# Kernel tuning notes

Measured on AMD Instinct MI355X. Metric: run time of the kernel, lower is better.

## Reference

```python
import jax, jax.numpy as jnp
import numpy as np

N, E, B = 20000, 320000, 64
IN_DIM, HID, HEADS, NGF = 128, 64, 4, 9
NEG_SLOPE = 0.2
SET2SET_STEPS = 3


def _gat_conv(x, src, dst, W, a_src, a_dst, b, n):
    # PyG GATConv (eval mode): h = xW split into heads, edge score =
    # LeakyReLU(a_src.h[src] + a_dst.h[dst]), softmax over edges per dst node,
    # weighted scatter-sum of h[src], heads concatenated, + bias.
    H, C = a_src.shape
    h = (x @ W).reshape(n, H, C)                       # [N,H,C]
    s = jnp.sum(h * a_src, axis=-1)                    # [N,H]
    d = jnp.sum(h * a_dst, axis=-1)                    # [N,H]
    e = jax.nn.leaky_relu(s[src] + d[dst], NEG_SLOPE)  # [E,H]
    emax = jax.ops.segment_max(e, dst, num_segments=n)
    ex = jnp.exp(e - emax[dst])
    denom = jax.ops.segment_sum(ex, dst, num_segments=n)
    alpha = ex / (denom[dst] + 1e-16)                  # [E,H]
    out = jax.ops.segment_sum(h[src] * alpha[..., None], dst, num_segments=n)
    return out.reshape(n, H * C) + b


def _set2set(x, batch, Wih, Whh, bih, bhh, n_graphs):
    # Set2Set pooling: LSTM(q_star) -> attention over nodes per graph -> readout.
    d = x.shape[1]
    h = jnp.zeros((n_graphs, d), x.dtype)
    c = jnp.zeros((n_graphs, d), x.dtype)
    q_star = jnp.zeros((n_graphs, 2 * d), x.dtype)
    for _ in range(SET2SET_STEPS):
        gates = q_star @ Wih.T + bih + h @ Whh.T + bhh   # [B,4d], torch gate order i,f,g,o
        i, f, g, o = jnp.split(gates, 4, axis=1)
        c = jax.nn.sigmoid(f) * c + jax.nn.sigmoid(i) * jnp.tanh(g)
        h = jax.nn.sigmoid(o) * jnp.tanh(c)
        q = h                                            # [B,d]
        e = jnp.sum(x * q[batch], axis=-1)               # [N]
        emax = jax.ops.segment_max(e, batch, num_segments=n_graphs)
        a = jnp.exp(e - emax[batch])
        a = a / (jax.ops.segment_sum(a, batch, num_segments=n_graphs)[batch] + 1e-16)
        r = jax.ops.segment_sum(a[:, None] * x, batch, num_segments=n_graphs)  # [B,d]
        q_star = jnp.concatenate([q, r], axis=1)
    return q_star


def setup_inputs() -> dict:
    key = jax.random.key(0)
    ks = jax.random.split(key, 20)
    sc = 0.1
    inp = {
        "x": jax.random.normal(ks[0], (N, IN_DIM), jnp.float32),
        "edge_index": jax.random.randint(ks[1], (2, E), 0, N, dtype=jnp.int32),
        "batch": jnp.sort(jax.random.randint(ks[2], (N,), 0, B, dtype=jnp.int32)),
        "graph_features": jax.random.normal(ks[3], (B, NGF), jnp.float32),
        "W1": sc * jax.random.normal(ks[4], (IN_DIM, HEADS * HID), jnp.float32),
        "a_src1": sc * jax.random.normal(ks[5], (HEADS, HID), jnp.float32),
        "a_dst1": sc * jax.random.normal(ks[6], (HEADS, HID), jnp.float32),
        "b1": jnp.zeros((HEADS * HID,), jnp.float32),
        "W2": sc * jax.random.normal(ks[7], (HEADS * HID, HEADS * HID), jnp.float32),
        "a_src2": sc * jax.random.normal(ks[8], (HEADS, HID), jnp.float32),
        "a_dst2": sc * jax.random.normal(ks[9], (HEADS, HID), jnp.float32),
        "b2": jnp.zeros((HEADS * HID,), jnp.float32),
        "W3": sc * jax.random.normal(ks[10], (HEADS * HID, 2 * HID), jnp.float32),
        "a_src3": sc * jax.random.normal(ks[11], (1, 2 * HID), jnp.float32),
        "a_dst3": sc * jax.random.normal(ks[12], (1, 2 * HID), jnp.float32),
        "b3": jnp.zeros((2 * HID,), jnp.float32),
        "Wih": sc * jax.random.normal(ks[13], (4 * 2 * HID, 4 * HID), jnp.float32),
        "Whh": sc * jax.random.normal(ks[14], (4 * 2 * HID, 2 * HID), jnp.float32),
        "bih": jnp.zeros((4 * 2 * HID,), jnp.float32),
        "bhh": jnp.zeros((4 * 2 * HID,), jnp.float32),
        "gW1": sc * jax.random.normal(ks[15], (NGF, HID), jnp.float32),
        "gb1": jnp.zeros((HID,), jnp.float32),
        "gW2": sc * jax.random.normal(ks[16], (HID, HID // 2), jnp.float32),
        "gb2": jnp.zeros((HID // 2,), jnp.float32),
        "mW1": sc * jax.random.normal(ks[17], (2 * (2 * HID) + HID // 2, 128), jnp.float32),
        "mb1": jnp.zeros((128,), jnp.float32),
        "mW2": sc * jax.random.normal(ks[18], (128, 4), jnp.float32),
        "mb2": jnp.zeros((4,), jnp.float32),
    }
    return inp


def reference(x, edge_index, batch, graph_features,
              W1, a_src1, a_dst1, b1,
              W2, a_src2, a_dst2, b2,
              W3, a_src3, a_dst3, b3,
              Wih, Whh, bih, bhh,
              gW1, gb1, gW2, gb2,
              mW1, mb1, mW2, mb2):
    n = x.shape[0]
    # PyG GATConv default add_self_loops=True
    loops = jnp.arange(n, dtype=edge_index.dtype)
    src = jnp.concatenate([edge_index[0], loops])
    dst = jnp.concatenate([edge_index[1], loops])
    h = jax.nn.elu(_gat_conv(x, src, dst, W1, a_src1, a_dst1, b1, n))
    h = jax.nn.elu(_gat_conv(h, src, dst, W2, a_src2, a_dst2, b2, n))
    h = jax.nn.elu(_gat_conv(h, src, dst, W3, a_src3, a_dst3, b3, n))
    pooled = _set2set(h, batch, Wih, Whh, bih, bhh, B)              # [B, 256]
    gf = jax.nn.relu(graph_features @ gW1 + gb1) @ gW2 + gb2        # [B, 32]
    z = jnp.concatenate([pooled, gf], axis=1)                       # [B, 288]
    scores = jax.nn.relu(z @ mW1 + mb1) @ mW2 + mb2                 # [B, 4]
    return scores
```

## Files before the change

### kernel.cpp

```cpp
#include <hip/hip_runtime.h>
#include <hip/hip_bf16.h>
#include <math.h>

#define NEG_SLOPE 0.2f

typedef __attribute__((ext_vector_type(8))) short bf16x8;
typedef __attribute__((ext_vector_type(4))) float f32x4;

__device__ __forceinline__ float sigmoidf(float x){ return 1.f/(1.f+expf(-x)); }

__device__ __forceinline__ unsigned pack_split(float v){
  __hip_bfloat16 hi = __float2bfloat16(v);
  float rem = v - __bfloat162float(hi);
  __hip_bfloat16 lo = __float2bfloat16(rem);
  unsigned short uh = __builtin_bit_cast(unsigned short, hi);
  unsigned short ul = __builtin_bit_cast(unsigned short, lo);
  return (unsigned)uh | ((unsigned)ul << 16);
}
__device__ __forceinline__ unsigned short bf16of(float v){
  __hip_bfloat16 h = __float2bfloat16(v);
  return __builtin_bit_cast(unsigned short, h);
}

__global__ void init_kernel(int* counts, int* gstart, int* gend,
                            float* rsum, float* lsum,
                            int* pad1, int* pad2, int npadints,
                            const float* __restrict__ W1, unsigned* __restrict__ WT1,
                            const float* __restrict__ W2, unsigned* __restrict__ WT2,
                            const float* __restrict__ W3, unsigned* __restrict__ WT3,
                            int n, int b){
  int i = blockIdx.x*blockDim.x + threadIdx.x;
  if (i < n) counts[i] = 0;
  if (i < b){ gstart[i] = 0; gend[i] = 0; }
  if (i < 3*b*128) rsum[i] = 0.f;
  if (i < 3*b) lsum[i] = 0.f;
  if (i < npadints){ pad1[i] = 0; pad2[i] = 0; }
  if (i < 128*256){
    int k = i>>8, c = i&255;
    WT1[(size_t)c*128 + k] = pack_split(W1[i]);
  }
  if (i < 256*256){
    int k = i>>8, c = i&255;
    WT2[(size_t)c*256 + k] = pack_split(W2[i]);
  }
  if (i < 256*128){
    int k = i>>7, c = i&127;
    WT3[(size_t)c*256 + k] = pack_split(W3[i]);
  }
}

__global__ void build_kernel(const int* __restrict__ ei, const int* __restrict__ batch,
                             int* counts, int* gstart, int* gend, int E, int n){
  int i = blockIdx.x*blockDim.x + threadIdx.x;
  if (i < E) atomicAdd(&counts[ei[E+i]], 1);
  if (i < n){
    int b = batch[i];
    if (i == 0 || batch[i-1] != b) gstart[b] = i;
    if (i == n-1 || batch[i+1] != b) gend[b] = i+1;
  }
}

__global__ void scan_kernel(const int* __restrict__ counts, int* offs, int* cursor, int n){
  const int T = 1024;
  int tid = threadIdx.x;
  int chunk = (n + T - 1)/T;
  int base = tid*chunk;
  int local = 0;
  for (int i=0;i<chunk;i++){ int idx=base+i; if (idx<n) local += counts[idx]; }
  __shared__ int ss[T];
  ss[tid]=local; __syncthreads();
  for (int off=1; off<T; off<<=1){
    int v = (tid>=off)? ss[tid-off] : 0;
    __syncthreads();
    ss[tid]+=v;
    __syncthreads();
  }
  int run = ss[tid]-local;
  for (int i=0;i<chunk;i++){
    int idx=base+i;
    if (idx<n){ offs[idx]=run; cursor[idx]=run; run += counts[idx]; }
  }
  if (tid==T-1) offs[n]=run;
}

__global__ void fill_kernel(const int* __restrict__ ei, int* cursor, int* csr, int E){
  int i = blockIdx.x*blockDim.x + threadIdx.x;
  if (i<E){
    int dst = ei[E+i];
    int pos = atomicAdd(&cursor[dst],1);
    csr[pos] = ei[i];
  }
}

template<bool AF32>
__global__ __launch_bounds__(256) void gemm_bf16(
    const void* __restrict__ Aptr, const short* __restrict__ BT,
    float* __restrict__ C, unsigned short* __restrict__ Cb16,
    int M, int Ktot, int N){
  __shared__ short As[64][72];
  __shared__ short Bs[128][72];
  int tid = threadIdx.x;
  int wave = tid>>6, lane = tid&63;
  int quad = lane>>4, l16 = lane&15;
  int bm = blockIdx.x*64, bn = blockIdx.y*128;
  f32x4 acc[8];
  #pragma unroll
  for (int i=0;i<8;i++) acc[i] = (f32x4){0.f,0.f,0.f,0.f};
  int rr = tid>>3;
  int seg = (tid&7)*8;
  int4 ra[2], rb[4];
  auto loadAB = [&](int k0){
    if (AF32){
      const float* A = (const float*)Aptr;
      int Kf = Ktot>>1;
      int fo = (k0+seg)>>1;
      #pragma unroll
      for (int p=0;p<2;p++){
        int row = bm + p*32 + rr;
        float4 v = make_float4(0.f,0.f,0.f,0.f);
        if (row < M) v = *(const float4*)(A + (size_t)row*Kf + fo);
        ra[p] = make_int4((int)pack_split(v.x),(int)pack_split(v.y),
                          (int)pack_split(v.z),(int)pack_split(v.w));
      }
    } else {
      const short* A = (const short*)Aptr;
      #pragma unroll
      for (int p=0;p<2;p++)
        ra[p] = *(const int4*)(A + (size_t)(bm + p*32 + rr)*Ktot + k0 + seg);
    }
    #pragma unroll
    for (int p=0;p<4;p++)
      rb[p] = *(const int4*)(BT + (size_t)(bn + p*32 + rr)*Ktot + k0 + seg);
  };
  loadAB(0);
  for (int k0=0; k0<Ktot; k0+=64){
    __syncthreads();
    #pragma unroll
    for (int p=0;p<2;p++) *(int4*)&As[p*32+rr][seg] = ra[p];
    #pragma unroll
    for (int p=0;p<4;p++) *(int4*)&Bs[p*32+rr][seg] = rb[p];
    __syncthreads();
    if (k0+64 < Ktot) loadAB(k0+64);
    #pragma unroll
    for (int kk=0;kk<2;kk++){
      bf16x8 af = *(bf16x8*)&As[wave*16 + l16][kk*32 + quad*8];
      #pragma unroll
      for (int nf=0;nf<8;nf++){
        bf16x8 bfv = *(bf16x8*)&Bs[nf*16 + l16][kk*32 + quad*8];
        acc[nf] = __builtin_amdgcn_mfma_f32_16x16x32_bf16(af, bfv, acc[nf], 0,0,0);
      }
    }
  }
  #pragma unroll
  for (int r=0;r<4;r++){
    int row = bm + wave*16 + quad*4 + r;
    if (row < M){
      #pragma unroll
      for (int nf=0;nf<8;nf++){
        float v = acc[nf][r];
        int col = bn + nf*16 + l16;
        C[(size_t)row*N + col] = v;
        Cb16[(size_t)row*N + col] = bf16of(v);
      }
    }
  }
}

template<int H, int C>
__global__ void sd_kernel(const float* __restrict__ h, const float* __restrict__ asrc,
                          const float* __restrict__ adst, float* __restrict__ s,
                          float* __restrict__ d, int n_nodes){
  constexpr int HC = H*C;
  int wave = threadIdx.x >> 6, lane = threadIdx.x & 63;
  int n = blockIdx.x*4 + wave;
  if (n >= n_nodes) return;
  if (HC == 256){
    float4 hv = *reinterpret_cast<const float4*>(h + (size_t)n*256 + lane*4);
    float4 av = *reinterpret_cast<const float4*>(asrc + lane*4);
    float4 dv = *reinterpret_cast<const float4*>(adst + lane*4);
    float ps = hv.x*av.x + hv.y*av.y + hv.z*av.z + hv.w*av.w;
    float pd = hv.x*dv.x + hv.y*dv.y + hv.z*dv.z + hv.w*dv.w;
    #pragma unroll
    for (int off=1; off<16; off<<=1){ ps += __shfl_xor(ps,off); pd += __shfl_xor(pd,off); }
    if ((lane&15)==0){
      int head = lane>>4;
      s[n*4+head]=ps; d[n*4+head]=pd;
    }
  } else {
    if (lane < 32){
      float4 hv = *reinterpret_cast<const float4*>(h + (size_t)n*128 + lane*4);
      float4 av = *reinterpret_cast<const float4*>(asrc + lane*4);
      float4 dv = *reinterpret_cast<const float4*>(adst + lane*4);
      float ps = hv.x*av.x + hv.y*av.y + hv.z*av.z + hv.w*av.w;
      float pd = hv.x*dv.x + hv.y*dv.y + hv.z*dv.z + hv.w*dv.w;
      #pragma unroll
      for (int off=1; off<32; off<<=1){ ps += __shfl_xor(ps,off); pd += __shfl_xor(pd,off); }
      if (lane==0){ s[n]=ps; d[n]=pd; }
    }
  }
}

template<int H, int C, bool SPLIT>
__global__ __launch_bounds__(256) void agg_kernel(
    const unsigned short* __restrict__ hb, const float* __restrict__ s,
    const float* __restrict__ d, const int* __restrict__ offs,
    const int* __restrict__ csr, const float* __restrict__ bias,
    float* __restrict__ yf, unsigned* __restrict__ ys, int n_nodes){
  constexpr int HC = H*C;
  constexpr int VEC = HC/64;
  int n = blockIdx.x;
  int tid = threadIdx.x;
  int wave = tid>>6, lane = tid&63;
  __shared__ float sdst[H];
  __shared__ float sl[H];
  __shared__ float sw[64*H];
  __shared__ int ssrc[64];
  __shared__ float facc[4][HC];
  if (tid < H) sdst[tid] = d[n*H+tid];
  int start = offs[n];
  int cnt = offs[n+1]-start;
  int cnt1 = cnt+1;
  __syncthreads();
  float acc[VEC] = {};
  float lp[H];
  #pragma unroll
  for (int h=0;h<H;h++) lp[h]=0.f;
  for (int base=0; base<cnt1; base+=64){
    int nchunk = min(64, cnt1-base);
    if (tid < nchunk){
      int i = base+tid;
      int src = (i==cnt) ? n : csr[start+i];
      ssrc[tid]=src;
      if (H == 4){
        float4 sv = *reinterpret_cast<const float4*>(s + (size_t)src*4);
        float ev[4] = {sv.x, sv.y, sv.z, sv.w};
        #pragma unroll
        for (int h=0;h<4;h++){
          float e = ev[h] + sdst[h];
          e = e>=0.f ? e : NEG_SLOPE*e;
          float w = expf(e);
          sw[tid*4+h]=w;
          lp[h]+=w;
        }
      } else {
        float e = s[src] + sdst[0];
        e = e>=0.f ? e : NEG_SLOPE*e;
        float w = expf(e);
        sw[tid]=w;
        lp[0]+=w;
      }
    }
    __syncthreads();
    for (int j=wave; j<nchunk; j+=4){
      int src = ssrc[j];
      const unsigned short* hp = hb + (size_t)src*HC + lane*VEC;
      if (VEC == 4){
        float wt = sw[j*H + (lane>>4)];
        int2 hv = *reinterpret_cast<const int2*>(hp);
        acc[0] += wt*__uint_as_float(((unsigned)hv.x & 0xFFFFu) << 16);
        acc[1] += wt*__uint_as_float((unsigned)hv.x & 0xFFFF0000u);
        acc[2] += wt*__uint_as_float(((unsigned)hv.y & 0xFFFFu) << 16);
        acc[3] += wt*__uint_as_float((unsigned)hv.y & 0xFFFF0000u);
      } else {
        float wt = sw[j];
        unsigned hv = *reinterpret_cast<const unsigned*>(hp);
        acc[0] += wt*__uint_as_float((hv & 0xFFFFu) << 16);
        acc[1] += wt*__uint_as_float(hv & 0xFFFF0000u);
      }
    }
    __syncthreads();
  }
  if (wave==0){
    #pragma unroll
    for (int off=32; off; off>>=1)
      #pragma unroll
      for (int h=0;h<H;h++) lp[h] += __shfl_down(lp[h],off);
    if (lane==0)
      #pragma unroll
      for (int h=0;h<H;h++) sl[h]=lp[h];
  }
  #pragma unroll
  for (int v=0;v<VEC;v++) facc[wave][lane*VEC+v] = acc[v];
  __syncthreads();
  if (tid < HC){
    float a = facc[0][tid]+facc[1][tid]+facc[2][tid]+facc[3][tid];
    int head = tid / C;
    float o = a/(sl[head]+1e-16f) + bias[tid];
    o = o>0.f ? o : expm1f(o);
    if (SPLIT){
      ys[(size_t)n*HC + tid] = pack_split(o);
    } else {
      yf[(size_t)n*HC + tid] = o;
    }
  }
}

__global__ __launch_bounds__(256) void read_kernel(
    const float* __restrict__ x, const float* __restrict__ q,
    const int* __restrict__ batch,
    float* __restrict__ rsum, float* __restrict__ lsum, int N){
  int tid = threadIdx.x;
  int wave = tid>>6, lane = tid&63;
  int c0 = blockIdx.x*32;
  if (c0 >= N) return;
  __shared__ float ws[32];
  __shared__ int gb[32];
  if (tid < 32 && c0+tid < N) gb[tid] = batch[c0+tid];
  __syncthreads();
  #pragma unroll
  for (int j=0;j<8;j++){
    int k = wave*8 + j;
    int i = c0 + k;
    if (i < N){
      int g = gb[k];
      float2 xv = *reinterpret_cast<const float2*>(x + (size_t)i*128 + lane*2);
      float2 qv = *reinterpret_cast<const float2*>(q + (size_t)g*128 + lane*2);
      float p = xv.x*qv.x + xv.y*qv.y;
      #pragma unroll
      for (int off=32; off; off>>=1) p += __shfl_down(p, off);
      if (lane==0) ws[k] = expf(p);
    }
  }
  __syncthreads();
  if (tid < 128){
    int col = tid;
    int endi = min(c0+32, N);
    int curg = gb[0];
    float acc = 0.f, lacc = 0.f;
    for (int i=c0; i<endi; ++i){
      int g = gb[i-c0];
      if (g != curg){
        atomicAdd(&rsum[curg*128+col], acc);
        if (col==0) atomicAdd(&lsum[curg], lacc);
        acc = 0.f; lacc = 0.f; curg = g;
      }
      float w = ws[i-c0];
      acc += w * x[(size_t)i*128+col];
      lacc += w;
    }
    atomicAdd(&rsum[curg*128+col], acc);
    if (col==0) atomicAdd(&lsum[curg], lacc);
  }
}

template<int STEP>
__global__ __launch_bounds__(256) void s2s_step_kernel(
    const float* __restrict__ rsum, const float* __restrict__ lsum,
    float* __restrict__ hc, float* __restrict__ qbuf,
    const float* __restrict__ Wih, const float* __restrict__ Whh,
    const float* __restrict__ bih, const float* __restrict__ bhh,
    const float* __restrict__ gfeat,
    const float* __restrict__ gW1, const float* __restrict__ gb1,
    const float* __restrict__ gW2, const float* __restrict__ gb2,
    const float* __restrict__ mW1, const float* __restrict__ mb1,
    const float* __restrict__ mW2, const float* __restrict__ mb2,
    float* __restrict__ out, int B){
  int b = blockIdx.x, tid = threadIdx.x;
  __shared__ float qs[256];

  if (STEP > 0){
    if (tid < 128){
      const float* rs = rsum + (size_t)(STEP-1)*B*128 + (size_t)b*128;
      float ls = lsum[(STEP-1)*B + b];
      qs[tid]     = qbuf[b*128+tid];
      qs[128+tid] = rs[tid] / (ls + 1e-16f);
    }
    __syncthreads();
  }

  if (STEP < 3){
    __shared__ float hs[128], gsh[512];
    if (STEP > 0){ if (tid<128) hs[tid] = hc[(size_t)b*128+tid]; }
    __syncthreads();
    #pragma unroll
    for (int p=0;p<2;p++){
      int j = tid + p*256;
      float a = bih[j] + bhh[j];
      if (STEP > 0){
        const float* wi = Wih + (size_t)j*256;
        for (int k=0;k<256;k+=4)
          a += qs[k]*wi[k] + qs[k+1]*wi[k+1] + qs[k+2]*wi[k+2] + qs[k+3]*wi[k+3];
        const float* wh = Whh + (size_t)j*128;
        for (int k=0;k<128;k+=4)
          a += hs[k]*wh[k] + hs[k+1]*wh[k+1] + hs[k+2]*wh[k+2] + hs[k+3]*wh[k+3];
      }
      gsh[j] = a;
    }
    __syncthreads();
    if (tid < 128){
      float cprev = (STEP==0) ? 0.f : hc[(size_t)(B+b)*128+tid];
      float ig = sigmoidf(gsh[tid]);
      float fg = sigmoidf(gsh[128+tid]);
      float gg = tanhf(gsh[256+tid]);
      float og = sigmoidf(gsh[384+tid]);
      float c2 = fg*cprev + ig*gg;
      float h2 = og*tanhf(c2);
      hc[(size_t)b*128+tid] = h2;
      hc[(size_t)(B+b)*128+tid] = c2;
      qbuf[b*128+tid] = h2;
    }
  } else {
    __shared__ float z[288], gf1[64], hid[128];
    z[tid] = qs[tid];
    if (tid < 64){
      float a = gb1[tid];
      for (int k=0;k<9;k++) a += gfeat[b*9+k]*gW1[k*64+tid];
      gf1[tid] = a>0.f ? a : 0.f;
    }
    __syncthreads();
    if (tid < 32){
      float a = gb2[tid];
      for (int k=0;k<64;k++) a += gf1[k]*gW2[k*32+tid];
      z[256+tid] = a;
    }
    __syncthreads();
    if (tid < 128){
      float a = mb1[tid];
      for (int k=0;k<288;k++) a += z[k]*mW1[(size_t)k*128+tid];
      hid[tid] = a>0.f ? a : 0.f;
    }
    __syncthreads();
    if (tid < 4){
      float a = mb2[tid];
      for (int k=0;k<128;k++) a += hid[k]*mW2[k*4+tid];
      out[b*4+tid] = a;
    }
  }
}

extern "C" void kernel_launch(void* const* d_in, const int* in_sizes, int n_in,
                              void* d_out, int out_size, void* d_ws, size_t ws_size,
                              hipStream_t stream) {
  const float* x     = (const float*)d_in[0];
  const int*   ei    = (const int*)d_in[1];
  const int*   batch = (const int*)d_in[2];
  const float* gfeat = (const float*)d_in[3];
  const float* W1    = (const float*)d_in[4];
  const float* as1   = (const float*)d_in[5];
  const float* ad1   = (const float*)d_in[6];
  const float* b1    = (const float*)d_in[7];
  const float* W2    = (const float*)d_in[8];
  const float* as2   = (const float*)d_in[9];
  const float* ad2   = (const float*)d_in[10];
  const float* b2    = (const float*)d_in[11];
  const float* W3    = (const float*)d_in[12];
  const float* as3   = (const float*)d_in[13];
  const float* ad3   = (const float*)d_in[14];
  const float* b3    = (const float*)d_in[15];
  const float* Wih   = (const float*)d_in[16];
  const float* Whh   = (const float*)d_in[17];
  const float* bih   = (const float*)d_in[18];
  const float* bhh   = (const float*)d_in[19];
  const float* gW1   = (const float*)d_in[20];
  const float* gb1   = (const float*)d_in[21];
  const float* gW2   = (const float*)d_in[22];
  const float* gb2   = (const float*)d_in[23];
  const float* mW1   = (const float*)d_in[24];
  const float* mb1   = (const float*)d_in[25];
  const float* mW2   = (const float*)d_in[26];
  const float* mb2   = (const float*)d_in[27];

  const int N = in_sizes[0]/128;
  const int E = in_sizes[1]/2;
  const int B = in_sizes[3]/9;
  const int Mpad = ((N + 127)/128)*128;

  char* ws = (char*)d_ws;
  size_t off = 0;
  auto alloc = [&](size_t bytes)->char*{
    char* p = ws + off;
    off += (bytes + 255) & ~(size_t)255;
    return p;
  };
  float*    hbuf    = (float*)alloc((size_t)N*256*4);
  unsigned short* hb16 = (unsigned short*)alloc((size_t)N*256*2);
  unsigned* ysplit1 = (unsigned*)alloc((size_t)Mpad*256*4);
  unsigned* ysplit2 = (unsigned*)alloc((size_t)Mpad*256*4);
  float*    ybuf    = (float*)alloc((size_t)N*128*4);
  unsigned* WT1     = (unsigned*)alloc((size_t)256*128*4);
  unsigned* WT2     = (unsigned*)alloc((size_t)256*256*4);
  unsigned* WT3     = (unsigned*)alloc((size_t)128*256*4);
  float* sbuf   = (float*)alloc((size_t)N*4*4);
  float* dbuf   = (float*)alloc((size_t)N*4*4);
  int*   counts = (int*)alloc((size_t)N*4);
  int*   offs   = (int*)alloc((size_t)(N+1)*4);
  int*   cursor = (int*)alloc((size_t)N*4);
  int*   csr    = (int*)alloc((size_t)E*4);
  int*   gstart = (int*)alloc((size_t)B*4);
  int*   gend   = (int*)alloc((size_t)B*4);
  float* hcbuf  = (float*)alloc((size_t)2*B*128*4);
  float* qbuf   = (float*)alloc((size_t)B*128*4);
  float* rsum   = (float*)alloc((size_t)3*B*128*4);
  float* lsum   = (float*)alloc((size_t)3*B*4);

  int npadints = (Mpad - N)*256;
  int nInit = max(max(N, npadints), 256*256);
  init_kernel<<<(nInit+255)/256, 256, 0, stream>>>(counts, gstart, gend,
      rsum, lsum, (int*)(ysplit1 + (size_t)N*256), (int*)(ysplit2 + (size_t)N*256),
      npadints, W1, WT1, W2, WT2, W3, WT3, N, B);
  int gridEN = (max(E,N)+255)/256;
  build_kernel<<<gridEN, 256, 0, stream>>>(ei, batch, counts, gstart, gend, E, N);
  scan_kernel<<<1, 1024, 0, stream>>>(counts, offs, cursor, N);
  fill_kernel<<<(E+255)/256, 256, 0, stream>>>(ei, cursor, csr, E);

  int gm = Mpad/64;
  gemm_bf16<true><<<dim3(gm,2), 256, 0, stream>>>((const void*)x, (const short*)WT1,
                                                  hbuf, hb16, N, 256, 256);
  sd_kernel<4,64><<<(N+3)/4, 256, 0, stream>>>(hbuf, as1, ad1, sbuf, dbuf, N);
  agg_kernel<4,64,true><<<N, 256, 0, stream>>>(hb16, sbuf, dbuf, offs, csr, b1, nullptr, ysplit1, N);
  gemm_bf16<false><<<dim3(gm,2), 256, 0, stream>>>((const void*)ysplit1, (const short*)WT2,
                                                   hbuf, hb16, N, 512, 256);
  sd_kernel<4,64><<<(N+3)/4, 256, 0, stream>>>(hbuf, as2, ad2, sbuf, dbuf, N);
  agg_kernel<4,64,true><<<N, 256, 0, stream>>>(hb16, sbuf, dbuf, offs, csr, b2, nullptr, ysplit2, N);
  gemm_bf16<false><<<dim3(gm,1), 256, 0, stream>>>((const void*)ysplit2, (const short*)WT3,
                                                   hbuf, hb16, N, 512, 128);
  sd_kernel<1,128><<<(N+3)/4, 256, 0, stream>>>(hbuf, as3, ad3, sbuf, dbuf, N);
  agg_kernel<1,128,false><<<N, 256, 0, stream>>>(hb16, sbuf, dbuf, offs, csr, b3, ybuf, nullptr, N);

  int gr = (N+31)/32;
  s2s_step_kernel<0><<<B, 256, 0, stream>>>(rsum, lsum, hcbuf, qbuf,
      Wih, Whh, bih, bhh, gfeat, gW1, gb1, gW2, gb2, mW1, mb1, mW2, mb2, (float*)d_out, B);
  read_kernel<<<gr, 256, 0, stream>>>(ybuf, qbuf, batch, rsum + 0*(size_t)B*128, lsum + 0*B, N);
  s2s_step_kernel<1><<<B, 256, 0, stream>>>(rsum, lsum, hcbuf, qbuf,
      Wih, Whh, bih, bhh, gfeat, gW1, gb1, gW2, gb2, mW1, mb1, mW2, mb2, (float*)d_out, B);
  read_kernel<<<gr, 256, 0, stream>>>(ybuf, qbuf, batch, rsum + 1*(size_t)B*128, lsum + 1*B, N);
  s2s_step_kernel<2><<<B, 256, 0, stream>>>(rsum, lsum, hcbuf, qbuf,
      Wih, Whh, bih, bhh, gfeat, gW1, gb1, gW2, gb2, mW1, mb1, mW2, mb2, (float*)d_out, B);
  read_kernel<<<gr, 256, 0, stream>>>(ybuf, qbuf, batch, rsum + 2*(size_t)B*128, lsum + 2*B, N);
  s2s_step_kernel<3><<<B, 256, 0, stream>>>(rsum, lsum, hcbuf, qbuf,
      Wih, Whh, bih, bhh, gfeat, gW1, gb1, gW2, gb2, mW1, mb1, mW2, mb2, (float*)d_out, B);
}
```

Measured before the change: 531.9 us.

## Drop fp32 GEMM output, stage bf16 stores through LDS, compute scores from bf16

The GEMM no longer writes an fp32 copy of h. It writes only bf16, staged through shared memory so each row is stored as coalesced 32-bit words instead of scattered 16-bit stores. The attention-score kernel now reads the bf16 h, which halves its traffic, and the grid axes are swapped so the column blocks of a row tile run next to each other. The cost is that the attention scores s and d are now computed from rounded bf16 values, which reduces their precision.

```diff
diff --git a/kernel.cpp b/kernel.cpp
--- a/kernel.cpp
+++ b/kernel.cpp
@@ -8,6 +8,7 @@
 typedef __attribute__((ext_vector_type(4))) float f32x4;
 
 __device__ __forceinline__ float sigmoidf(float x){ return 1.f/(1.f+expf(-x)); }
+__device__ __forceinline__ float bf2f(unsigned us){ return __uint_as_float(us << 16); }
 
 __device__ __forceinline__ unsigned pack_split(float v){
   __hip_bfloat16 hi = __float2bfloat16(v);
@@ -95,14 +96,13 @@
 template<bool AF32>
 __global__ __launch_bounds__(256) void gemm_bf16(
     const void* __restrict__ Aptr, const short* __restrict__ BT,
-    float* __restrict__ C, unsigned short* __restrict__ Cb16,
-    int M, int Ktot, int N){
+    unsigned short* __restrict__ Cb16, int M, int Ktot, int N){
   __shared__ short As[64][72];
   __shared__ short Bs[128][72];
   int tid = threadIdx.x;
   int wave = tid>>6, lane = tid&63;
   int quad = lane>>4, l16 = lane&15;
-  int bm = blockIdx.x*64, bn = blockIdx.y*128;
+  int bm = blockIdx.y*64, bn = blockIdx.x*128;
   f32x4 acc[8];
   #pragma unroll
   for (int i=0;i<8;i++) acc[i] = (f32x4){0.f,0.f,0.f,0.f};
@@ -151,35 +151,41 @@
       }
     }
   }
+  __syncthreads();
+  unsigned short* stg = (unsigned short*)(&As[0][0]) + wave*528;
   #pragma unroll
   for (int r=0;r<4;r++){
-    int row = bm + wave*16 + quad*4 + r;
-    if (row < M){
-      #pragma unroll
-      for (int nf=0;nf<8;nf++){
-        float v = acc[nf][r];
-        int col = bn + nf*16 + l16;
-        C[(size_t)row*N + col] = v;
-        Cb16[(size_t)row*N + col] = bf16of(v);
+    #pragma unroll
+    for (int nf=0;nf<8;nf++)
+      stg[quad*132 + nf*16 + l16] = bf16of(acc[nf][r]);
+    #pragma unroll
+    for (int p=0;p<4;p++){
+      int row = bm + wave*16 + p*4 + r;
+      if (row < M){
+        unsigned v = (unsigned)stg[p*132 + lane*2] |
+                     ((unsigned)stg[p*132 + lane*2 + 1] << 16);
+        *(unsigned*)(Cb16 + (size_t)row*N + bn + lane*2) = v;
       }
     }
   }
 }
 
 template<int H, int C>
-__global__ void sd_kernel(const float* __restrict__ h, const float* __restrict__ asrc,
+__global__ void sd_kernel(const unsigned short* __restrict__ hb,
+                          const float* __restrict__ asrc,
                           const float* __restrict__ adst, float* __restrict__ s,
                           float* __restrict__ d, int n_nodes){
-  constexpr int HC = H*C;
   int wave = threadIdx.x >> 6, lane = threadIdx.x & 63;
   int n = blockIdx.x*4 + wave;
   if (n >= n_nodes) return;
-  if (HC == 256){
-    float4 hv = *reinterpret_cast<const float4*>(h + (size_t)n*256 + lane*4);
+  if (H == 4){
+    uint2 u = *reinterpret_cast<const uint2*>(hb + (size_t)n*256 + lane*4);
     float4 av = *reinterpret_cast<const float4*>(asrc + lane*4);
     float4 dv = *reinterpret_cast<const float4*>(adst + lane*4);
-    float ps = hv.x*av.x + hv.y*av.y + hv.z*av.z + hv.w*av.w;
-    float pd = hv.x*dv.x + hv.y*dv.y + hv.z*dv.z + hv.w*dv.w;
+    float h0 = bf2f(u.x & 0xFFFFu), h1 = bf2f(u.x >> 16);
+    float h2 = bf2f(u.y & 0xFFFFu), h3 = bf2f(u.y >> 16);
+    float ps = h0*av.x + h1*av.y + h2*av.z + h3*av.w;
+    float pd = h0*dv.x + h1*dv.y + h2*dv.z + h3*dv.w;
     #pragma unroll
     for (int off=1; off<16; off<<=1){ ps += __shfl_xor(ps,off); pd += __shfl_xor(pd,off); }
     if ((lane&15)==0){
@@ -187,16 +193,15 @@
       s[n*4+head]=ps; d[n*4+head]=pd;
     }
   } else {
-    if (lane < 32){
-      float4 hv = *reinterpret_cast<const float4*>(h + (size_t)n*128 + lane*4);
-      float4 av = *reinterpret_cast<const float4*>(asrc + lane*4);
-      float4 dv = *reinterpret_cast<const float4*>(adst + lane*4);
-      float ps = hv.x*av.x + hv.y*av.y + hv.z*av.z + hv.w*av.w;
-      float pd = hv.x*dv.x + hv.y*dv.y + hv.z*dv.z + hv.w*dv.w;
-      #pragma unroll
-      for (int off=1; off<32; off<<=1){ ps += __shfl_xor(ps,off); pd += __shfl_xor(pd,off); }
-      if (lane==0){ s[n]=ps; d[n]=pd; }
-    }
+    unsigned u = *reinterpret_cast<const unsigned*>(hb + (size_t)n*128 + lane*2);
+    float2 av = *reinterpret_cast<const float2*>(asrc + lane*2);
+    float2 dv = *reinterpret_cast<const float2*>(adst + lane*2);
+    float h0 = bf2f(u & 0xFFFFu), h1 = bf2f(u >> 16);
+    float ps = h0*av.x + h1*av.y;
+    float pd = h0*dv.x + h1*dv.y;
+    #pragma unroll
+    for (int off=1; off<64; off<<=1){ ps += __shfl_xor(ps,off); pd += __shfl_xor(pd,off); }
+    if (lane==0){ s[n]=ps; d[n]=pd; }
   }
 }
 
@@ -257,15 +262,15 @@
       if (VEC == 4){
         float wt = sw[j*H + (lane>>4)];
         int2 hv = *reinterpret_cast<const int2*>(hp);
-        acc[0] += wt*__uint_as_float(((unsigned)hv.x & 0xFFFFu) << 16);
-        acc[1] += wt*__uint_as_float((unsigned)hv.x & 0xFFFF0000u);
-        acc[2] += wt*__uint_as_float(((unsigned)hv.y & 0xFFFFu) << 16);
-        acc[3] += wt*__uint_as_float((unsigned)hv.y & 0xFFFF0000u);
+        acc[0] += wt*bf2f((unsigned)hv.x & 0xFFFFu);
+        acc[1] += wt*bf2f((unsigned)hv.x >> 16);
+        acc[2] += wt*bf2f((unsigned)hv.y & 0xFFFFu);
+        acc[3] += wt*bf2f((unsigned)hv.y >> 16);
       } else {
         float wt = sw[j];
         unsigned hv = *reinterpret_cast<const unsigned*>(hp);
-        acc[0] += wt*__uint_as_float((hv & 0xFFFFu) << 16);
-        acc[1] += wt*__uint_as_float(hv & 0xFFFF0000u);
+        acc[0] += wt*bf2f(hv & 0xFFFFu);
+        acc[1] += wt*bf2f(hv >> 16);
       }
     }
     __syncthreads();
@@ -472,7 +477,6 @@
     off += (bytes + 255) & ~(size_t)255;
     return p;
   };
-  float*    hbuf    = (float*)alloc((size_t)N*256*4);
   unsigned short* hb16 = (unsigned short*)alloc((size_t)N*256*2);
   unsigned* ysplit1 = (unsigned*)alloc((size_t)Mpad*256*4);
   unsigned* ysplit2 = (unsigned*)alloc((size_t)Mpad*256*4);
@@ -504,17 +508,17 @@
   fill_kernel<<<(E+255)/256, 256, 0, stream>>>(ei, cursor, csr, E);
 
   int gm = Mpad/64;
-  gemm_bf16<true><<<dim3(gm,2), 256, 0, stream>>>((const void*)x, (const short*)WT1,
-                                                  hbuf, hb16, N, 256, 256);
-  sd_kernel<4,64><<<(N+3)/4, 256, 0, stream>>>(hbuf, as1, ad1, sbuf, dbuf, N);
+  gemm_bf16<true><<<dim3(2,gm), 256, 0, stream>>>((const void*)x, (const short*)WT1,
+                                                  hb16, N, 256, 256);
+  sd_kernel<4,64><<<(N+3)/4, 256, 0, stream>>>(hb16, as1, ad1, sbuf, dbuf, N);
   agg_kernel<4,64,true><<<N, 256, 0, stream>>>(hb16, sbuf, dbuf, offs, csr, b1, nullptr, ysplit1, N);
-  gemm_bf16<false><<<dim3(gm,2), 256, 0, stream>>>((const void*)ysplit1, (const short*)WT2,
-                                                   hbuf, hb16, N, 512, 256);
-  sd_kernel<4,64><<<(N+3)/4, 256, 0, stream>>>(hbuf, as2, ad2, sbuf, dbuf, N);
+  gemm_bf16<false><<<dim3(2,gm), 256, 0, stream>>>((const void*)ysplit1, (const short*)WT2,
+                                                   hb16, N, 512, 256);
+  sd_kernel<4,64><<<(N+3)/4, 256, 0, stream>>>(hb16, as2, ad2, sbuf, dbuf, N);
   agg_kernel<4,64,true><<<N, 256, 0, stream>>>(hb16, sbuf, dbuf, offs, csr, b2, nullptr, ysplit2, N);
-  gemm_bf16<false><<<dim3(gm,1), 256, 0, stream>>>((const void*)ysplit2, (const short*)WT3,
-                                                   hbuf, hb16, N, 512, 128);
-  sd_kernel<1,128><<<(N+3)/4, 256, 0, stream>>>(hbuf, as3, ad3, sbuf, dbuf, N);
+  gemm_bf16<false><<<dim3(1,gm), 256, 0, stream>>>((const void*)ysplit2, (const short*)WT3,
+                                                   hb16, N, 512, 128);
+  sd_kernel<1,128><<<(N+3)/4, 256, 0, stream>>>(hb16, as3, ad3, sbuf, dbuf, N);
   agg_kernel<1,128,false><<<N, 256, 0, stream>>>(hb16, sbuf, dbuf, offs, csr, b3, ybuf, nullptr, N);
 
   int gr = (N+31)/32;
```

Measured after the change: 526.8 us. No clear change (-1.0%).
